# Kernel tuning notes

Measured on AMD Instinct MI355X. Metric: run time of the kernel, lower is better.

Reference implementation:

```python
import jax, jax.numpy as jnp
import numpy as np

DIM = 1024
HID = 2816
N_ROUTED = 7  # num_experts - num_shared_experts
TOPK = 2
B, S = 4, 2048


def _expert(x, wg, wu, wd):
    # DeepSeekExpertLayer: down(silu(gate(x)) * up(x)); weights stored [in, out]
    return (jax.nn.silu(x @ wg) * (x @ wu)) @ wd


def setup_inputs() -> dict:
    key = jax.random.key(0)
    ks = jax.random.split(key, 9)
    s = 0.02
    x = jax.random.normal(ks[0], (B, S, DIM), jnp.float32)
    shared_gate = jax.random.normal(ks[1], (DIM, HID), jnp.float32) * s
    shared_up = jax.random.normal(ks[2], (DIM, HID), jnp.float32) * s
    shared_down = jax.random.normal(ks[3], (HID, DIM), jnp.float32) * s
    routed_gate = jax.random.normal(ks[4], (N_ROUTED, DIM, HID), jnp.float32) * s
    routed_up = jax.random.normal(ks[5], (N_ROUTED, DIM, HID), jnp.float32) * s
    routed_down = jax.random.normal(ks[6], (N_ROUTED, HID, DIM), jnp.float32) * s
    Wr = jax.random.normal(ks[7], (DIM, N_ROUTED), jnp.float32) * s
    # NOTE: original inits routing_bias to zeros (degenerate routing since logits
    # are MULTIPLIED by it); use random values so routing is non-trivial.
    routing_bias = jax.random.normal(ks[8], (N_ROUTED,), jnp.float32)
    return dict(x=x, shared_gate=shared_gate, shared_up=shared_up, shared_down=shared_down,
                routed_gate=routed_gate, routed_up=routed_up, routed_down=routed_down,
                Wr=Wr, routing_bias=routing_bias)


def reference(x, shared_gate, shared_up, shared_down,
              routed_gate, routed_up, routed_down, Wr, routing_bias):
    b, s, d = x.shape
    n_exp = routed_gate.shape[0]
    # shared expert path (num_shared_experts == 1, no division)
    shared_out = _expert(x, shared_gate, shared_up, shared_down)
    # router: note logits are MULTIPLIED by routing_bias (faithful to source)
    logits = (x @ Wr) * routing_bias            # [b, s, E]
    probs = jax.nn.sigmoid(logits)
    scores, idx = jax.lax.top_k(probs, TOPK)    # [b, s, k]
    scores = scores / scores.sum(-1, keepdims=True)
    # per-token per-expert combine weight via scatter-add of top-k scores
    t = b * s
    xf = x.reshape(t, d)
    weights = jnp.zeros((t, n_exp), x.dtype).at[
        jnp.arange(t)[:, None], idx.reshape(t, TOPK)].add(scores.reshape(t, TOPK))
    combined = jnp.zeros_like(xf)
    for e in range(n_exp):  # static small loop over experts
        combined = combined + _expert(xf, routed_gate[e], routed_up[e], routed_down[e]) * weights[:, e:e + 1]
    return shared_out + combined.reshape(b, s, d)
```

## Files before the change

kernel.cpp:

```cpp
#include <hip/hip_runtime.h>
#include <hip/hip_bf16.h>

#define DIM 1024
#define HID 2816
#define NEXP 7
#define TOKENS 8192

#define MW_XB    0ull
#define MW_H     16777216ull
#define MW_WGU   114098176ull
#define MW_WD    206372864ull
#define MW_TOK   252510208ull
#define MW_WGT   252579328ull
#define MW_META  252648448ull
#define MW_NEED  252650496ull

typedef __bf16 bf16x8 __attribute__((ext_vector_type(8)));
typedef float f32x4 __attribute__((ext_vector_type(4)));

static __device__ __forceinline__ unsigned short f2b(float f) {
  union { float f; unsigned int i; } c; c.f = f;
  unsigned int i = c.i;
  unsigned int r = (i + 0x7fffu + ((i >> 16) & 1u)) >> 16;
  return (unsigned short)r;
}

static __device__ __forceinline__ void gload16(const void* g, void* l) {
  __builtin_amdgcn_global_load_lds(
      (const __attribute__((address_space(1))) unsigned int*)g,
      (__attribute__((address_space(3))) unsigned int*)l, 16, 0, 0);
}

__global__ __launch_bounds__(256, 2) void router_kernel(
    const float* __restrict__ X,
    const float* __restrict__ Wr,
    const float* __restrict__ bias,
    int* __restrict__ eidx,
    float* __restrict__ ew)
{
// ... 8 lines not shown
  for (int d0 = 0; d0 < DIM; d0 += 4) {
    float4 xv = *(const float4*)(xp + d0);
    const float* xs = (const float*)&xv;
#pragma unroll
    for (int j = 0; j < 4; ++j) {
      float xf = xs[j];
#pragma unroll
      for (int e = 0; e < NEXP; ++e) acc[e] += xf * wr[(d0 + j) * NEXP + e];
    }
  }
  float p[NEXP];
#pragma unroll
  for (int e = 0; e < NEXP; ++e)
    p[e] = 1.f / (1.f + __expf(-acc[e] * bias[e]));
  float best = -1.f; int bi = 0;
#pragma unroll
  for (int e = 0; e < NEXP; ++e) if (p[e] > best) { best = p[e]; bi = e; }
  float sec = -1.f; int si = 0;
#pragma unroll
  for (int e = 0; e < NEXP; ++e) if (e != bi && p[e] > sec) { sec = p[e]; si = e; }
  float s = best + sec;
  eidx[t] = bi | (si << 8);
  ((float2*)ew)[t] = make_float2(best / s, sec / s);
}

__global__ __launch_bounds__(256) void build_kernel(
    const int* __restrict__ eidx, const float* __restrict__ ew,
    int* __restrict__ tok, float* __restrict__ wgt, int* __restrict__ meta,
    int padmode)
{
  __shared__ int cnt[NEXP], fill[NEXP], ofs[NEXP];
  if (threadIdx.x < NEXP) { cnt[threadIdx.x] = 0; fill[threadIdx.x] = 0; }
  __syncthreads();
  for (int t = threadIdx.x; t < TOKENS; t += 256) {
    int p = eidx[t];
    atomicAdd(&cnt[p & 0xff], 1);
    atomicAdd(&cnt[(p >> 8) & 0xff], 1);
  }
  __syncthreads();
  if (threadIdx.x == 0) {
    int o = 0, nb = 0;
    for (int e = 0; e < NEXP; ++e) {
      ofs[e] = o;
      meta[e] = cnt[e];
      meta[8 + e] = o;
      if (padmode) {
        int b = (cnt[e] + 127) >> 7;
        for (int i = 0; i < b; ++i) meta[16 + nb++] = e | (i << 3);
        o += b << 7;
      } else {
        o += cnt[e];
      }
    }
    meta[15] = nb;
  }
  __syncthreads();
  for (int t = threadIdx.x; t < TOKENS; t += 256) {
    int p = eidx[t];
    int e0 = p & 0xff, e1 = (p >> 8) & 0xff;
    float2 w = ((const float2*)ew)[t];
    int p0 = ofs[e0] + atomicAdd(&fill[e0], 1);
    tok[p0] = t; wgt[p0] = w.x;
    int p1 = ofs[e1] + atomicAdd(&fill[e1], 1);
    tok[p1] = t; wgt[p1] = w.y;
  }
}

__global__ __launch_bounds__(256) void xcvt_kernel(
    const float* __restrict__ X, unsigned short* __restrict__ Xb)
{
  int i = (blockIdx.x * 256 + threadIdx.x) * 8;
  float4 v0 = *(const float4*)&X[i];
  float4 v1 = *(const float4*)&X[i + 4];
  unsigned short o[8];
  o[0] = f2b(v0.x); o[1] = f2b(v0.y); o[2] = f2b(v0.z); o[3] = f2b(v0.w);
  o[4] = f2b(v1.x); o[5] = f2b(v1.y); o[6] = f2b(v1.z); o[7] = f2b(v1.w);
  *(int4*)&Xb[i] = *(const int4*)o;
}

__global__ __launch_bounds__(256) void transpose_all_kernel(
    const float* __restrict__ sg, const float* __restrict__ su, const float* __restrict__ sd,
    const float* __restrict__ rg, const float* __restrict__ ru, const float* __restrict__ rd,
    unsigned short* __restrict__ WguA, unsigned short* __restrict__ WdA)
{
  int b = blockIdx.x;
  int e = b / 2112, r = b % 2112;
  int m = r / 704, q2 = r % 704;
  const float* src; unsigned short* dst; int K, N, nb, kb;
  if (m == 0) {
    src = e ? rg + (size_t)(e - 1) * DIM * HID : sg;
    dst = WguA + (size_t)e * (2 * (size_t)HID * DIM);
    K = DIM; N = HID; nb = q2 % 44; kb = q2 / 44;
  } else if (m == 1) {
    src = e ? ru + (size_t)(e - 1) * DIM * HID : su;
    dst = WguA + (size_t)e * (2 * (size_t)HID * DIM) + (size_t)HID * DIM;
    K = DIM; N = HID; nb = q2 % 44; kb = q2 / 44;
  } else {
    src = e ? rd + (size_t)(e - 1) * HID * DIM : sd;
    dst = WdA + (size_t)e * ((size_t)HID * DIM);
    K = HID; N = DIM; nb = q2 % 16; kb = q2 / 16;
  }
  __shared__ unsigned short t[64][72];
  const int n0 = nb * 64, k0 = kb * 64;
  const int tid = threadIdx.x;
  const int kl = tid >> 4, nl = (tid & 15) * 4;
#pragma unroll
  for (int i = 0; i < 4; ++i) {
    int k = kl + i * 16;
    float4 v = *(const float4*)&src[(size_t)(k0 + k) * N + n0 + nl];
    t[nl + 0][k] = f2b(v.x); t[nl + 1][k] = f2b(v.y);
    t[nl + 2][k] = f2b(v.z); t[nl + 3][k] = f2b(v.w);
  }
  __syncthreads();
  const int nl2 = tid >> 3, kc = (tid & 7) * 8;
#pragma unroll
  for (int i = 0; i < 2; ++i) {
    int n = nl2 + i * 32;
    *(int4*)&dst[(size_t)(n0 + n) * K + k0 + kc] = *(const int4*)&t[n][kc];
  }
}


__global__ __launch_bounds__(256, 2) void gateup_kernel(
    const unsigned short* __restrict__ Xb,
    const unsigned short* __restrict__ Wgu,
    unsigned short* __restrict__ H)
{
  __shared__ __align__(16) unsigned short As[128 * 64];
  __shared__ __align__(16) unsigned short Bgs[64 * 64];
  __shared__ __align__(16) unsigned short Bus[64 * 64];
  const int m0 = blockIdx.y * 128;
  const int n0 = blockIdx.x * 64;
  const int tid = threadIdx.x;
  const int lane = tid & 63;
  const int w = tid >> 6;
  const int wm = (w & 1) * 64;
  const int wn = (w >> 1) * 32;
  const int c = lane & 15;
  const int q = lane >> 4;
  const int cx = c & 7;

  const unsigned short* Wg = Wgu;
  const unsigned short* Wu = Wgu + (size_t)HID * DIM;

  const int r8 = lane >> 3;
  const int swz = ((lane & 7) ^ r8) * 8;
  const int wrow = w * 8 + r8;

  const unsigned short* aptr[4];
#pragma unroll
  for (int i = 0; i < 4; ++i)
    aptr[i] = Xb + (size_t)(m0 + i * 32 + wrow) * DIM + swz;
  const unsigned short* gptr[2];
  const unsigned short* uptr[2];
#pragma unroll
  for (int i = 0; i < 2; ++i) {
    gptr[i] = Wg + (size_t)(n0 + i * 32 + wrow) * DIM + swz;
    uptr[i] = Wu + (size_t)(n0 + i * 32 + wrow) * DIM + swz;
  }

  f32x4 accg[4][2], accu[4][2];
#pragma unroll
  for (int mi = 0; mi < 4; ++mi)
#pragma unroll
    for (int ni = 0; ni < 2; ++ni) {
      accg[mi][ni] = {0.f, 0.f, 0.f, 0.f};
      accu[mi][ni] = {0.f, 0.f, 0.f, 0.f};
    }

  for (int k0 = 0; k0 < DIM; k0 += 64) {
    __syncthreads();
#pragma unroll
    for (int i = 0; i < 4; ++i) gload16(aptr[i] + k0, &As[i * 2048 + tid * 8]);
#pragma unroll
    for (int i = 0; i < 2; ++i) {
      gload16(gptr[i] + k0, &Bgs[i * 2048 + tid * 8]);
      gload16(uptr[i] + k0, &Bus[i * 2048 + tid * 8]);
    }
    __syncthreads();
#pragma unroll
    for (int h = 0; h < 2; ++h) {
      const int go = ((h * 4 + q) ^ cx) * 8;
      bf16x8 a[4], bg[2], bu[2];
#pragma unroll
      for (int mi = 0; mi < 4; ++mi)
        a[mi] = *(const bf16x8*)&As[(wm + mi * 16 + c) * 64 + go];
#pragma unroll
      for (int ni = 0; ni < 2; ++ni) {
        bg[ni] = *(const bf16x8*)&Bgs[(wn + ni * 16 + c) * 64 + go];
        bu[ni] = *(const bf16x8*)&Bus[(wn + ni * 16 + c) * 64 + go];
      }
#pragma unroll
// ... 14 lines not shown
        int row = wm + mi * 16 + q * 4 + r;
        int col = wn + ni * 16 + c;
        float g = accg[mi][ni][r];
        float u = accu[mi][ni][r];
        float h = (g / (1.f + __expf(-g))) * u;
        H[(size_t)(m0 + row) * HID + n0 + col] = f2b(h);
      }
}

__global__ __launch_bounds__(256, 2) void gateup_sparse_all_kernel(
    const unsigned short* __restrict__ Xb,
    const unsigned short* __restrict__ WguR,
    const int* __restrict__ tok, const float* __restrict__ wgt,
    const int* __restrict__ meta,
    unsigned short* __restrict__ H)
{
  const int yb = blockIdx.y;
  if (yb >= meta[15]) return;
  const int bm = meta[16 + yb];
  const int e = bm & 7, mb = bm >> 3;
  const int cnt = meta[e];
  const int pofs = meta[8 + e];
  const unsigned short* Wgu = WguR + (size_t)e * (2 * (size_t)HID * DIM);

  __shared__ __align__(16) unsigned short As[128 * 64];
  __shared__ __align__(16) unsigned short Bgs[64 * 64];
  __shared__ __align__(16) unsigned short Bus[64 * 64];
  __shared__ float wl[128];

  const int n0 = blockIdx.x * 64;
  const int tid = threadIdx.x;
  const int lane = tid & 63;
  const int w = tid >> 6;
  const int wm = (w & 1) * 64;
  const int wn = (w >> 1) * 32;
  const int c = lane & 15;
  const int q = lane >> 4;
  const int cx = c & 7;

  if (tid < 128)
    wl[tid] = (mb * 128 + tid < cnt) ? wgt[pofs + mb * 128 + tid] : 0.f;

  const unsigned short* Wg = Wgu;
  const unsigned short* Wu = Wgu + (size_t)HID * DIM;

  const int r8 = lane >> 3;
  const int swz = ((lane & 7) ^ r8) * 8;
  const int wrow = w * 8 + r8;

  const unsigned short* aptr[4];
#pragma unroll
  for (int i = 0; i < 4; ++i) {
    int s = mb * 128 + i * 32 + wrow;
    int t = (s < cnt) ? tok[pofs + s] : 0;
    aptr[i] = Xb + (size_t)t * DIM + swz;
  }
  const unsigned short* gptr[2];
  const unsigned short* uptr[2];
#pragma unroll
  for (int i = 0; i < 2; ++i) {
    gptr[i] = Wg + (size_t)(n0 + i * 32 + wrow) * DIM + swz;
    uptr[i] = Wu + (size_t)(n0 + i * 32 + wrow) * DIM + swz;
  }

  f32x4 accg[4][2], accu[4][2];
#pragma unroll
  for (int mi = 0; mi < 4; ++mi)
#pragma unroll
    for (int ni = 0; ni < 2; ++ni) {
      accg[mi][ni] = {0.f, 0.f, 0.f, 0.f};
      accu[mi][ni] = {0.f, 0.f, 0.f, 0.f};
    }

  for (int k0 = 0; k0 < DIM; k0 += 64) {
    __syncthreads();
#pragma unroll
    for (int i = 0; i < 4; ++i) gload16(aptr[i] + k0, &As[i * 2048 + tid * 8]);
#pragma unroll
    for (int i = 0; i < 2; ++i) {
      gload16(gptr[i] + k0, &Bgs[i * 2048 + tid * 8]);
      gload16(uptr[i] + k0, &Bus[i * 2048 + tid * 8]);
    }
    __syncthreads();
#pragma unroll
    for (int h = 0; h < 2; ++h) {
      const int go = ((h * 4 + q) ^ cx) * 8;
      bf16x8 a[4], bg[2], bu[2];
#pragma unroll
      for (int mi = 0; mi < 4; ++mi)
        a[mi] = *(const bf16x8*)&As[(wm + mi * 16 + c) * 64 + go];
#pragma unroll
      for (int ni = 0; ni < 2; ++ni) {
        bg[ni] = *(const bf16x8*)&Bgs[(wn + ni * 16 + c) * 64 + go];
        bu[ni] = *(const bf16x8*)&Bus[(wn + ni * 16 + c) * 64 + go];
      }
#pragma unroll
// ... 17 lines not shown
        float u = accu[mi][ni][r];
        float h = (g / (1.f + __expf(-g))) * u * wl[row];
        H[(size_t)(pofs + mb * 128 + row) * HID + n0 + col] = f2b(h);
      }
}

__global__ __launch_bounds__(256, 2) void down_dense_kernel(
    const unsigned short* __restrict__ Hm,
    const unsigned short* __restrict__ WdT,
    float* __restrict__ out)
{
  __shared__ __align__(16) unsigned short As[128 * 64];
  __shared__ __align__(16) unsigned short Bs[128 * 64];
  const int m0 = blockIdx.y * 128;
  const int n0 = blockIdx.x * 128;
  const int tid = threadIdx.x;
  const int lane = tid & 63;
  const int w4 = tid >> 6;
  const int wm = (w4 & 1) * 64;
  const int wn = (w4 >> 1) * 64;
  const int c = lane & 15;
  const int q = lane >> 4;
  const int cx = c & 7;

  const int r8 = lane >> 3;
  const int swz = ((lane & 7) ^ r8) * 8;
  const int wrow = w4 * 8 + r8;

  const unsigned short* aptr[4];
  const unsigned short* bptr[4];
#pragma unroll
  for (int i = 0; i < 4; ++i) {
    aptr[i] = Hm + (size_t)(m0 + i * 32 + wrow) * HID + swz;
    bptr[i] = WdT + (size_t)(n0 + i * 32 + wrow) * HID + swz;
  }

  f32x4 acc[4][4];
#pragma unroll
  for (int mi = 0; mi < 4; ++mi)
#pragma unroll
    for (int ni = 0; ni < 4; ++ni) acc[mi][ni] = {0.f, 0.f, 0.f, 0.f};

  for (int k0 = 0; k0 < HID; k0 += 64) {
    __syncthreads();
#pragma unroll
    for (int i = 0; i < 4; ++i) {
      gload16(aptr[i] + k0, &As[i * 2048 + tid * 8]);
      gload16(bptr[i] + k0, &Bs[i * 2048 + tid * 8]);
    }
    __syncthreads();
#pragma unroll
    for (int h = 0; h < 2; ++h) {
      const int go = ((h * 4 + q) ^ cx) * 8;
      bf16x8 a[4], b[4];
#pragma unroll
      for (int mi = 0; mi < 4; ++mi)
        a[mi] = *(const bf16x8*)&As[(wm + mi * 16 + c) * 64 + go];
#pragma unroll
      for (int ni = 0; ni < 4; ++ni)
        b[ni] = *(const bf16x8*)&Bs[(wn + ni * 16 + c) * 64 + go];
#pragma unroll
      for (int mi = 0; mi < 4; ++mi)
#pragma unroll
        for (int ni = 0; ni < 4; ++ni)
          acc[mi][ni] = __builtin_amdgcn_mfma_f32_16x16x32_bf16(a[mi], b[ni], acc[mi][ni], 0, 0, 0);
// ... 6 lines not shown
      int trow = m0 + wm + mi * 16 + q * 4 + r;
#pragma unroll
      for (int ni = 0; ni < 4; ++ni) {
        int col = n0 + wn + ni * 16 + c;
        out[(size_t)trow * DIM + col] = acc[mi][ni][r];
      }
    }
}

__global__ __launch_bounds__(256, 2) void down_sparse_all_kernel(
    const unsigned short* __restrict__ Hm,
    const unsigned short* __restrict__ WdR,
    const int* __restrict__ tok, const int* __restrict__ meta,
    float* __restrict__ out)
{
  const int yb = blockIdx.y;
  if (yb >= meta[15]) return;
  const int bm = meta[16 + yb];
  const int e = bm & 7, mb = bm >> 3;
  const int cnt = meta[e];
  const int pofs = meta[8 + e];
  const unsigned short* WdT = WdR + (size_t)e * ((size_t)HID * DIM);
  const int kbase = blockIdx.z * (HID / 2);

  __shared__ __align__(16) unsigned short As[128 * 64];
  __shared__ __align__(16) unsigned short Bs[128 * 64];
  __shared__ int tl[128];
  const int n0 = blockIdx.x * 128;
  const int tid = threadIdx.x;
  const int lane = tid & 63;
  const int w4 = tid >> 6;
  const int wm = (w4 & 1) * 64;
  const int wn = (w4 >> 1) * 64;
  const int c = lane & 15;
  const int q = lane >> 4;
  const int cx = c & 7;

  if (tid < 128)
    tl[tid] = (mb * 128 + tid < cnt) ? tok[pofs + mb * 128 + tid] : 0;

  const int r8 = lane >> 3;
  const int swz = ((lane & 7) ^ r8) * 8;
  const int wrow = w4 * 8 + r8;

  const unsigned short* aptr[4];
  const unsigned short* bptr[4];
#pragma unroll
  for (int i = 0; i < 4; ++i) {
    aptr[i] = Hm + (size_t)(pofs + mb * 128 + i * 32 + wrow) * HID + kbase + swz;
    bptr[i] = WdT + (size_t)(n0 + i * 32 + wrow) * HID + kbase + swz;
  }

  f32x4 acc[4][4];
#pragma unroll
  for (int mi = 0; mi < 4; ++mi)
#pragma unroll
    for (int ni = 0; ni < 4; ++ni) acc[mi][ni] = {0.f, 0.f, 0.f, 0.f};

  for (int k0 = 0; k0 < HID / 2; k0 += 64) {
    __syncthreads();
#pragma unroll
    for (int i = 0; i < 4; ++i) {
      gload16(aptr[i] + k0, &As[i * 2048 + tid * 8]);
      gload16(bptr[i] + k0, &Bs[i * 2048 + tid * 8]);
    }
    __syncthreads();
#pragma unroll
    for (int h = 0; h < 2; ++h) {
      const int go = ((h * 4 + q) ^ cx) * 8;
      bf16x8 a[4], b[4];
#pragma unroll
      for (int mi = 0; mi < 4; ++mi)
        a[mi] = *(const bf16x8*)&As[(wm + mi * 16 + c) * 64 + go];
#pragma unroll
      for (int ni = 0; ni < 4; ++ni)
        b[ni] = *(const bf16x8*)&Bs[(wn + ni * 16 + c) * 64 + go];
#pragma unroll
      for (int mi = 0; mi < 4; ++mi)
#pragma unroll
        for (int ni = 0; ni < 4; ++ni)
          acc[mi][ni] = __builtin_amdgcn_mfma_f32_16x16x32_bf16(a[mi], b[ni], acc[mi][ni], 0, 0, 0);
    }
  }
#pragma unroll
  for (int mi = 0; mi < 4; ++mi)
#pragma unroll
    for (int r = 0; r < 4; ++r) {
      int lr = wm + mi * 16 + q * 4 + r;
      if (mb * 128 + lr < cnt) {
        int t = tl[lr];
#pragma unroll
        for (int ni = 0; ni < 4; ++ni) {
          int col = n0 + wn + ni * 16 + c;
          atomicAdd(&out[(size_t)t * DIM + col], acc[mi][ni][r]);
        }
      }
    }
}

__global__ __launch_bounds__(256, 2) void gateup_sparse_kernel(
    const unsigned short* __restrict__ Xb,
    const unsigned short* __restrict__ Wgu,
    const int* __restrict__ tok, const float* __restrict__ wgt,
    const int* __restrict__ cntofs, int e,
    unsigned short* __restrict__ H)
{
  const int cnt = cntofs[e];
  const int mb = blockIdx.y;
  if (mb * 128 >= cnt) return;
  const int ofs = cntofs[8 + e];

  __shared__ __align__(16) unsigned short As[128 * 64];
  __shared__ __align__(16) unsigned short Bgs[64 * 64];
  __shared__ __align__(16) unsigned short Bus[64 * 64];
  __shared__ float wl[128];

  const int n0 = blockIdx.x * 64;
  const int tid = threadIdx.x;
  const int lane = tid & 63;
  const int w = tid >> 6;
  const int wm = (w & 1) * 64;
  const int wn = (w >> 1) * 32;
  const int c = lane & 15;
  const int q = lane >> 4;
  const int cx = c & 7;

  if (tid < 128)
    wl[tid] = (mb * 128 + tid < cnt) ? wgt[ofs + mb * 128 + tid] : 0.f;

  const unsigned short* Wg = Wgu;
  const unsigned short* Wu = Wgu + (size_t)HID * DIM;

  const int r8 = lane >> 3;
  const int swz = ((lane & 7) ^ r8) * 8;
  const int wrow = w * 8 + r8;

  const unsigned short* aptr[4];
#pragma unroll
  for (int i = 0; i < 4; ++i) {
    int s = mb * 128 + i * 32 + wrow;
    int t = (s < cnt) ? tok[ofs + s] : 0;
    aptr[i] = Xb + (size_t)t * DIM + swz;
  }
  const unsigned short* gptr[2];
  const unsigned short* uptr[2];
#pragma unroll
  for (int i = 0; i < 2; ++i) {
    gptr[i] = Wg + (size_t)(n0 + i * 32 + wrow) * DIM + swz;
    uptr[i] = Wu + (size_t)(n0 + i * 32 + wrow) * DIM + swz;
  }

  f32x4 accg[4][2], accu[4][2];
#pragma unroll
  for (int mi = 0; mi < 4; ++mi)
#pragma unroll
    for (int ni = 0; ni < 2; ++ni) {
      accg[mi][ni] = {0.f, 0.f, 0.f, 0.f};
      accu[mi][ni] = {0.f, 0.f, 0.f, 0.f};
    }

  for (int k0 = 0; k0 < DIM; k0 += 64) {
    __syncthreads();
#pragma unroll
    for (int i = 0; i < 4; ++i) gload16(aptr[i] + k0, &As[i * 2048 + tid * 8]);
#pragma unroll
    for (int i = 0; i < 2; ++i) {
      gload16(gptr[i] + k0, &Bgs[i * 2048 + tid * 8]);
      gload16(uptr[i] + k0, &Bus[i * 2048 + tid * 8]);
    }
    __syncthreads();
#pragma unroll
    for (int h = 0; h < 2; ++h) {
      const int go = ((h * 4 + q) ^ cx) * 8;
      bf16x8 a[4], bg[2], bu[2];
#pragma unroll
      for (int mi = 0; mi < 4; ++mi)
        a[mi] = *(const bf16x8*)&As[(wm + mi * 16 + c) * 64 + go];
#pragma unroll
      for (int ni = 0; ni < 2; ++ni) {
        bg[ni] = *(const bf16x8*)&Bgs[(wn + ni * 16 + c) * 64 + go];
        bu[ni] = *(const bf16x8*)&Bus[(wn + ni * 16 + c) * 64 + go];
      }
#pragma unroll
      for (int mi = 0; mi < 4; ++mi)
#pragma unroll
        for (int ni = 0; ni < 2; ++ni) {
          accg[mi][ni] = __builtin_amdgcn_mfma_f32_16x16x32_bf16(a[mi], bg[ni], accg[mi][ni], 0, 0, 0);
          accu[mi][ni] = __builtin_amdgcn_mfma_f32_16x16x32_bf16(a[mi], bu[ni], accu[mi][ni], 0, 0, 0);
        }
    }
  }
#pragma unroll
  for (int mi = 0; mi < 4; ++mi)
#pragma unroll
    for (int ni = 0; ni < 2; ++ni)
#pragma unroll
      for (int r = 0; r < 4; ++r) {
        int row = wm + mi * 16 + q * 4 + r;
        int col = wn + ni * 16 + c;
        float g = accg[mi][ni][r];
        float u = accu[mi][ni][r];
        float h = (g / (1.f + __expf(-g))) * u * wl[row];
        H[(size_t)(mb * 128 + row) * HID + n0 + col] = f2b(h);
      }
}

__global__ __launch_bounds__(256, 2) void down_sparse_kernel(
    const unsigned short* __restrict__ Hm,
    const unsigned short* __restrict__ WdT,
    const int* __restrict__ tok, const int* __restrict__ cntofs, int e,
    float* __restrict__ out)
{
  const int cnt = cntofs[e];
  const int mb = blockIdx.y;
  if (mb * 128 >= cnt) return;
  const int ofs = cntofs[8 + e];
  const int kbase = blockIdx.z * (HID / 2);

  __shared__ __align__(16) unsigned short As[128 * 64];
  __shared__ __align__(16) unsigned short Bs[128 * 64];
  __shared__ int tl[128];
  const int n0 = blockIdx.x * 128;
  const int tid = threadIdx.x;
  const int lane = tid & 63;
  const int w4 = tid >> 6;
  const int wm = (w4 & 1) * 64;
  const int wn = (w4 >> 1) * 64;
  const int c = lane & 15;
  const int q = lane >> 4;
  const int cx = c & 7;

  if (tid < 128)
    tl[tid] = (mb * 128 + tid < cnt) ? tok[ofs + mb * 128 + tid] : 0;

  const int r8 = lane >> 3;
  const int swz = ((lane & 7) ^ r8) * 8;
  const int wrow = w4 * 8 + r8;

  const unsigned short* aptr[4];
  const unsigned short* bptr[4];
#pragma unroll
  for (int i = 0; i < 4; ++i) {
    aptr[i] = Hm + (size_t)(mb * 128 + i * 32 + wrow) * HID + kbase + swz;
    bptr[i] = WdT + (size_t)(n0 + i * 32 + wrow) * HID + kbase + swz;
  }

  f32x4 acc[4][4];
#pragma unroll
  for (int mi = 0; mi < 4; ++mi)
#pragma unroll
    for (int ni = 0; ni < 4; ++ni) acc[mi][ni] = {0.f, 0.f, 0.f, 0.f};

  for (int k0 = 0; k0 < HID / 2; k0 += 64) {
    __syncthreads();
#pragma unroll
    for (int i = 0; i < 4; ++i) {
      gload16(aptr[i] + k0, &As[i * 2048 + tid * 8]);
      gload16(bptr[i] + k0, &Bs[i * 2048 + tid * 8]);
    }
    __syncthreads();
#pragma unroll
    for (int h = 0; h < 2; ++h) {
      const int go = ((h * 4 + q) ^ cx) * 8;
      bf16x8 a[4], b[4];
#pragma unroll
      for (int mi = 0; mi < 4; ++mi)
        a[mi] = *(const bf16x8*)&As[(wm + mi * 16 + c) * 64 + go];
#pragma unroll
      for (int ni = 0; ni < 4; ++ni)
        b[ni] = *(const bf16x8*)&Bs[(wn + ni * 16 + c) * 64 + go];
#pragma unroll
      for (int mi = 0; mi < 4; ++mi)
#pragma unroll
        for (int ni = 0; ni < 4; ++ni)
          acc[mi][ni] = __builtin_amdgcn_mfma_f32_16x16x32_bf16(a[mi], b[ni], acc[mi][ni], 0, 0, 0);
// ... 13 lines not shown
        }
      }
    }
}

extern "C" void kernel_launch(void* const* d_in, const int* in_sizes, int n_in,
                              void* d_out, int out_size, void* d_ws, size_t ws_size,
                              hipStream_t stream) {
  (void)in_sizes; (void)n_in; (void)out_size;
  const float* x   = (const float*)d_in[0];
  const float* sg  = (const float*)d_in[1];
  const float* su  = (const float*)d_in[2];
  const float* sd  = (const float*)d_in[3];
  const float* rg  = (const float*)d_in[4];
  const float* ru  = (const float*)d_in[5];
  const float* rd  = (const float*)d_in[6];
  const float* wrr = (const float*)d_in[7];
  const float* rb  = (const float*)d_in[8];
  float* out = (float*)d_out;

  char* ws = (char*)d_ws;
  dim3 blk(256);

  if (ws_size >= MW_NEED) {
    unsigned short* Xb   = (unsigned short*)(ws + MW_XB);
    unsigned short* H    = (unsigned short*)(ws + MW_H);
    unsigned short* WguA = (unsigned short*)(ws + MW_WGU);
    unsigned short* WdA  = (unsigned short*)(ws + MW_WD);
    int*   tok           = (int*)(ws + MW_TOK);
    float* wgt           = (float*)(ws + MW_WGT);
    int*   meta          = (int*)(ws + MW_META);
    int*   eidx = (int*)H;
    float* ew   = (float*)((char*)H + 32768);

    router_kernel<<<dim3(TOKENS / 256), blk, 0, stream>>>(x, wrr, rb, eidx, ew);
    xcvt_kernel<<<dim3(TOKENS * DIM / (8 * 256)), blk, 0, stream>>>(x, Xb);
    build_kernel<<<dim3(1), blk, 0, stream>>>(eidx, ew, tok, wgt, meta, 1);
    transpose_all_kernel<<<dim3(8 * 2112), blk, 0, stream>>>(sg, su, sd, rg, ru, rd, WguA, WdA);

    gateup_kernel<<<dim3(HID / 64, TOKENS / 128), blk, 0, stream>>>(Xb, WguA, H);
    down_dense_kernel<<<dim3(DIM / 128, TOKENS / 128), blk, 0, stream>>>(H, WdA, out);

    const unsigned short* WguRt = WguA + 2 * (size_t)HID * DIM;
    const unsigned short* WdRt  = WdA + (size_t)HID * DIM;
    gateup_sparse_all_kernel<<<dim3(HID / 64, 135), blk, 0, stream>>>(Xb, WguRt, tok, wgt, meta, H);
    down_sparse_all_kernel<<<dim3(DIM / 128, 135, 2), blk, 0, stream>>>(H, WdRt, tok, meta, out);
  } else {
    unsigned short* Xb  = (unsigned short*)ws;
    unsigned short* H   = (unsigned short*)(ws + 16777216);
    unsigned short* Wgu = (unsigned short*)(ws + 62914560);
    unsigned short* Wd  = (unsigned short*)(ws + 74448896);
    int*   tok          = (int*)(ws + 80216064);
    float* wgt          = (float*)(ws + 80281600);
    int*   meta         = (int*)(ws + 80347136);
    int*   eidx = (int*)H;
    float* ew   = (float*)((char*)H + 32768);

    router_kernel<<<dim3(TOKENS / 256), blk, 0, stream>>>(x, wrr, rb, eidx, ew);
    xcvt_kernel<<<dim3(TOKENS * DIM / (8 * 256)), blk, 0, stream>>>(x, Xb);
    build_kernel<<<dim3(1), blk, 0, stream>>>(eidx, ew, tok, wgt, meta, 0);

    dim3 ggu(HID / 64, TOKENS / 128);
    dim3 gdn(DIM / 128, TOKENS / 128);
    dim3 gdns(DIM / 128, TOKENS / 128, 2);

    for (int e = 0; e < 8; ++e) {
      const float* eg = (e == 0) ? sg : rg + (size_t)(e - 1) * DIM * HID;
      const float* eu = (e == 0) ? su : ru + (size_t)(e - 1) * DIM * HID;
      const float* ed = (e == 0) ? sd : rd + (size_t)(e - 1) * HID * DIM;
      transpose_all_kernel<<<dim3(2112), blk, 0, stream>>>(eg, eu, ed, eg, eu, ed, Wgu, Wd);
      if (e == 0) {
        gateup_kernel<<<ggu, blk, 0, stream>>>(Xb, Wgu, H);
        down_dense_kernel<<<gdn, blk, 0, stream>>>(H, Wd, out);
      } else {
        gateup_sparse_kernel<<<ggu, blk, 0, stream>>>(Xb, Wgu, tok, wgt, meta, e - 1, H);
        down_sparse_kernel<<<gdns, blk, 0, stream>>>(H, Wd, tok, meta, e - 1, out);
      }
    }
  }
}
```

Before: 946.7 us.

## Unify shared and routed experts into single grouped GEMMs with deterministic combine

Treats the shared expert as expert 0 with an identity token list, so one grouped gate/up kernel and one grouped down kernel cover all experts. Workgroup IDs are remapped across XCDs so neighbouring tiles share weights in cache. The down GEMM now writes per-slot fp32 partials instead of atomically accumulating into the output, and a separate combine kernel sums the shared and two routed partials per token. A wave-ballot build kernel fills slot tables. This cuts launch count and atomic traffic, at the cost of a larger workspace and an extra fp32 partial write and read.

```diff
diff --git a/kernel.cpp b/kernel.cpp
--- a/kernel.cpp
+++ b/kernel.cpp
@@ -5,6 +5,16 @@
 #define HID 2816
 #define NEXP 7
 #define TOKENS 8192
+
+#define MW2_XB    0ull
+#define MW2_WGU   16777216ull
+#define MW2_WD    109051904ull
+#define MW2_H     155189248ull
+#define MW2_TOK   298647552ull
+#define MW2_WGT   298749440ull
+#define MW2_SLT   298851328ull
+#define MW2_META  298916864ull
+#define MW2_NEED  298918912ull
 
 #define MW_XB    0ull
 #define MW_H     16777216ull
@@ -15,6 +25,9 @@
 #define MW_META  252648448ull
 #define MW_NEED  252650496ull
 
+#define GU_NWG (44 * 199)
+#define DN_NWG (8 * 199)
+
 typedef __bf16 bf16x8 __attribute__((ext_vector_type(8)));
 typedef float f32x4 __attribute__((ext_vector_type(4)));
 
@@ -69,48 +82,6 @@
   float s = best + sec;
   eidx[t] = bi | (si << 8);
   ((float2*)ew)[t] = make_float2(best / s, sec / s);
-}
-
-__global__ __launch_bounds__(256) void build_kernel(
-    const int* __restrict__ eidx, const float* __restrict__ ew,
-    int* __restrict__ tok, float* __restrict__ wgt, int* __restrict__ meta,
-    int padmode)
-{
-  __shared__ int cnt[NEXP], fill[NEXP], ofs[NEXP];
-  if (threadIdx.x < NEXP) { cnt[threadIdx.x] = 0; fill[threadIdx.x] = 0; }
-  __syncthreads();
-  for (int t = threadIdx.x; t < TOKENS; t += 256) {
-    int p = eidx[t];
-    atomicAdd(&cnt[p & 0xff], 1);
-    atomicAdd(&cnt[(p >> 8) & 0xff], 1);
-  }
-  __syncthreads();
-  if (threadIdx.x == 0) {
-    int o = 0, nb = 0;
-    for (int e = 0; e < NEXP; ++e) {
-      ofs[e] = o;
-      meta[e] = cnt[e];
-      meta[8 + e] = o;
-      if (padmode) {
-        int b = (cnt[e] + 127) >> 7;
-        for (int i = 0; i < b; ++i) meta[16 + nb++] = e | (i << 3);
-        o += b << 7;
-      } else {
-        o += cnt[e];
-      }
-    }
-    meta[15] = nb;
-  }
-  __syncthreads();
-  for (int t = threadIdx.x; t < TOKENS; t += 256) {
-    int p = eidx[t];
-    int e0 = p & 0xff, e1 = (p >> 8) & 0xff;
-    float2 w = ((const float2*)ew)[t];
-    int p0 = ofs[e0] + atomicAdd(&fill[e0], 1);
-    tok[p0] = t; wgt[p0] = w.x;
-    int p1 = ofs[e1] + atomicAdd(&fill[e1], 1);
-    tok[p1] = t; wgt[p1] = w.y;
-  }
 }
 
 __global__ __launch_bounds__(256) void xcvt_kernel(
@@ -123,6 +94,75 @@
   o[0] = f2b(v0.x); o[1] = f2b(v0.y); o[2] = f2b(v0.z); o[3] = f2b(v0.w);
   o[4] = f2b(v1.x); o[5] = f2b(v1.y); o[6] = f2b(v1.z); o[7] = f2b(v1.w);
   *(int4*)&Xb[i] = *(const int4*)o;
+}
+
+__global__ __launch_bounds__(256) void build2_kernel(
+    const int* __restrict__ eidx, const float* __restrict__ ew,
+    int* __restrict__ tok, float* __restrict__ wgt,
+    int2* __restrict__ slt, int* __restrict__ meta)
+{
+  __shared__ int cnt[NEXP], fill[NEXP], ofs[NEXP];
+  const int tid = threadIdx.x;
+  const int lane = tid & 63, wid = tid >> 6;
+  if (tid < NEXP) { cnt[tid] = 0; fill[tid] = 0; }
+  for (int i = tid; i < TOKENS; i += 256) { tok[i] = i; wgt[i] = 1.f; }
+  __syncthreads();
+  const unsigned long long lmask = (1ull << lane) - 1ull;
+  for (int base = wid * 64; base < TOKENS; base += 256) {
+    int t = base + lane;
+    int p = eidx[t];
+    int e0 = p & 0xff, e1 = (p >> 8) & 0xff;
+#pragma unroll
+    for (int e = 0; e < NEXP; ++e) {
+      unsigned long long m0 = __ballot(e0 == e);
+      unsigned long long m1 = __ballot(e1 == e);
+      if (lane == 0) {
+        int tot = __popcll(m0) + __popcll(m1);
+        if (tot) atomicAdd(&cnt[e], tot);
+      }
+    }
+  }
+  __syncthreads();
+  if (tid == 0) {
+    int o = 0, nb = 0;
+    meta[0] = TOKENS; meta[8] = 0;
+    for (int i = 0; i < TOKENS / 128; ++i) meta[17 + nb++] = 0 | (i << 4);
+    for (int e = 0; e < NEXP; ++e) {
+      ofs[e] = o;
+      meta[1 + e] = cnt[e];
+      meta[9 + e] = TOKENS + o;
+      int b = (cnt[e] + 127) >> 7;
+      for (int i = 0; i < b; ++i) meta[17 + nb++] = (e + 1) | (i << 4);
+      o += b << 7;
+    }
+    meta[16] = nb;
+  }
+  __syncthreads();
+  for (int base = wid * 64; base < TOKENS; base += 256) {
+    int t = base + lane;
+    int p = eidx[t];
+    int e0 = p & 0xff, e1 = (p >> 8) & 0xff;
+    float2 w = ((const float2*)ew)[t];
+    int s0 = 0, s1 = 0;
+#pragma unroll
+    for (int e = 0; e < NEXP; ++e) {
+      unsigned long long m0 = __ballot(e0 == e);
+      unsigned long long m1 = __ballot(e1 == e);
+      int tot = __popcll(m0) + __popcll(m1);
+      int wb = 0;
+      if (lane == 0 && tot) wb = atomicAdd(&fill[e], tot);
+      wb = __shfl(wb, 0);
+      if (e0 == e) {
+        int sl = TOKENS + ofs[e] + wb + __popcll(m0 & lmask);
+        tok[sl] = t; wgt[sl] = w.x; s0 = sl;
+      }
+      if (e1 == e) {
+        int sl = TOKENS + ofs[e] + wb + __popcll(m0) + __popcll(m1 & lmask);
+        tok[sl] = t; wgt[sl] = w.y; s1 = sl;
+      }
+    }
+    slt[t] = make_int2(s0, s1);
+  }
 }
 
 __global__ __launch_bounds__(256) void transpose_all_kernel(
@@ -168,6 +208,260 @@
 }
 
 
+__global__ __launch_bounds__(256, 2) void gateup_all_kernel(
+    const unsigned short* __restrict__ Xb,
+    const unsigned short* __restrict__ WguA,
+    const int* __restrict__ tok, const float* __restrict__ wgt,
+    const int* __restrict__ meta,
+    unsigned short* __restrict__ H)
+{
+  const int q8 = GU_NWG / 8, r8g = GU_NWG % 8;
+  const int id = blockIdx.x;
+  const int xcd = id & 7, pos = id >> 3;
+  const int sid = (xcd < r8g ? xcd * (q8 + 1) : r8g * (q8 + 1) + (xcd - r8g) * q8) + pos;
+  const int yb = sid / 44, nblk = sid - yb * 44;
+  if (yb >= meta[16]) return;
+  const int ent = meta[17 + yb];
+  const int e = ent & 15, mb = ent >> 4;
+  const int cnt = meta[e];
+  const int pofs = meta[8 + e];
+  const unsigned short* Wg = WguA + (size_t)e * (2 * (size_t)HID * DIM);
+  const unsigned short* Wu = Wg + (size_t)HID * DIM;
+
+  __shared__ __align__(16) unsigned short As[128 * 64];
+  __shared__ __align__(16) unsigned short Bgs[64 * 64];
+  __shared__ __align__(16) unsigned short Bus[64 * 64];
+  __shared__ float wl[128];
+
+  const int n0 = nblk * 64;
+  const int tid = threadIdx.x;
+  const int lane = tid & 63;
+  const int w = tid >> 6;
+  const int wm = (w & 1) * 64;
+  const int wn = (w >> 1) * 32;
+  const int c = lane & 15;
+  const int q = lane >> 4;
+  const int cx = c & 7;
+
+  if (tid < 128)
+    wl[tid] = (mb * 128 + tid < cnt) ? wgt[pofs + mb * 128 + tid] : 0.f;
+
+  const int r8 = lane >> 3;
+  const int swz = ((lane & 7) ^ r8) * 8;
+  const int wrow = w * 8 + r8;
+
+  const unsigned short* aptr[4];
+#pragma unroll
+  for (int i = 0; i < 4; ++i) {
+    int s = mb * 128 + i * 32 + wrow;
+    int t = (s < cnt) ? tok[pofs + s] : 0;
+    aptr[i] = Xb + (size_t)t * DIM + swz;
+  }
+  const unsigned short* gptr[2];
+  const unsigned short* uptr[2];
+#pragma unroll
+  for (int i = 0; i < 2; ++i) {
+    gptr[i] = Wg + (size_t)(n0 + i * 32 + wrow) * DIM + swz;
+    uptr[i] = Wu + (size_t)(n0 + i * 32 + wrow) * DIM + swz;
+  }
+
+  f32x4 accg[4][2], accu[4][2];
+#pragma unroll
+  for (int mi = 0; mi < 4; ++mi)
+#pragma unroll
+    for (int ni = 0; ni < 2; ++ni) {
+      accg[mi][ni] = {0.f, 0.f, 0.f, 0.f};
+      accu[mi][ni] = {0.f, 0.f, 0.f, 0.f};
+    }
+
+  for (int k0 = 0; k0 < DIM; k0 += 64) {
+    __syncthreads();
+#pragma unroll
+    for (int i = 0; i < 4; ++i) gload16(aptr[i] + k0, &As[i * 2048 + tid * 8]);
+#pragma unroll
+    for (int i = 0; i < 2; ++i) {
+      gload16(gptr[i] + k0, &Bgs[i * 2048 + tid * 8]);
+      gload16(uptr[i] + k0, &Bus[i * 2048 + tid * 8]);
+    }
+    __syncthreads();
+#pragma unroll
+    for (int h = 0; h < 2; ++h) {
+      const int go = ((h * 4 + q) ^ cx) * 8;
+      bf16x8 a[4], bg[2], bu[2];
+#pragma unroll
+      for (int mi = 0; mi < 4; ++mi)
+        a[mi] = *(const bf16x8*)&As[(wm + mi * 16 + c) * 64 + go];
+#pragma unroll
+      for (int ni = 0; ni < 2; ++ni) {
+        bg[ni] = *(const bf16x8*)&Bgs[(wn + ni * 16 + c) * 64 + go];
+        bu[ni] = *(const bf16x8*)&Bus[(wn + ni * 16 + c) * 64 + go];
+      }
+#pragma unroll
+      for (int mi = 0; mi < 4; ++mi)
+#pragma unroll
+        for (int ni = 0; ni < 2; ++ni) {
+          accg[mi][ni] = __builtin_amdgcn_mfma_f32_16x16x32_bf16(a[mi], bg[ni], accg[mi][ni], 0, 0, 0);
+          accu[mi][ni] = __builtin_amdgcn_mfma_f32_16x16x32_bf16(a[mi], bu[ni], accu[mi][ni], 0, 0, 0);
+        }
+    }
+  }
+#pragma unroll
+  for (int mi = 0; mi < 4; ++mi)
+#pragma unroll
+    for (int ni = 0; ni < 2; ++ni)
+#pragma unroll
+      for (int r = 0; r < 4; ++r) {
+        int row = wm + mi * 16 + q * 4 + r;
+        int col = wn + ni * 16 + c;
+        float g = accg[mi][ni][r];
+        float u = accu[mi][ni][r];
+        float h = (g / (1.f + __expf(-g))) * u * wl[row];
+        H[(size_t)(pofs + mb * 128 + row) * HID + n0 + col] = f2b(h);
+      }
+}
+
+__global__ __launch_bounds__(256, 2) void down_all_kernel(
+    const unsigned short* __restrict__ Hm,
+    const unsigned short* __restrict__ WdA,
+    const int* __restrict__ meta,
+    float* __restrict__ P)
+{
+  const int q8 = DN_NWG / 8;
+  const int id = blockIdx.x;
+  const int sid = (id & 7) * q8 + (id >> 3);
+  const int yb = sid >> 3, nblk = sid & 7;
+  if (yb >= meta[16]) return;
+  const int ent = meta[17 + yb];
+  const int e = ent & 15, mb = ent >> 4;
+  const int pofs = meta[8 + e];
+  const unsigned short* WdT = WdA + (size_t)e * ((size_t)HID * DIM);
+
+  __shared__ __align__(16) unsigned short As[128 * 64];
+  __shared__ __align__(16) unsigned short Bs[128 * 64];
+  const int n0 = nblk * 128;
+  const int tid = threadIdx.x;
+  const int lane = tid & 63;
+  const int w4 = tid >> 6;
+  const int wm = (w4 & 1) * 64;
+  const int wn = (w4 >> 1) * 64;
+  const int c = lane & 15;
+  const int q = lane >> 4;
+  const int cx = c & 7;
+
+  const int r8 = lane >> 3;
+  const int swz = ((lane & 7) ^ r8) * 8;
+  const int wrow = w4 * 8 + r8;
+
+  const unsigned short* aptr[4];
+  const unsigned short* bptr[4];
+#pragma unroll
+  for (int i = 0; i < 4; ++i) {
+    aptr[i] = Hm + (size_t)(pofs + mb * 128 + i * 32 + wrow) * HID + swz;
+    bptr[i] = WdT + (size_t)(n0 + i * 32 + wrow) * HID + swz;
+  }
+
+  f32x4 acc[4][4];
+#pragma unroll
+  for (int mi = 0; mi < 4; ++mi)
+#pragma unroll
+    for (int ni = 0; ni < 4; ++ni) acc[mi][ni] = {0.f, 0.f, 0.f, 0.f};
+
+  for (int k0 = 0; k0 < HID; k0 += 64) {
+    __syncthreads();
+#pragma unroll
+    for (int i = 0; i < 4; ++i) {
+      gload16(aptr[i] + k0, &As[i * 2048 + tid * 8]);
+      gload16(bptr[i] + k0, &Bs[i * 2048 + tid * 8]);
+    }
+    __syncthreads();
+#pragma unroll
+    for (int h = 0; h < 2; ++h) {
+      const int go = ((h * 4 + q) ^ cx) * 8;
+      bf16x8 a[4], b[4];
+#pragma unroll
+      for (int mi = 0; mi < 4; ++mi)
+        a[mi] = *(const bf16x8*)&As[(wm + mi * 16 + c) * 64 + go];
+#pragma unroll
+      for (int ni = 0; ni < 4; ++ni)
+        b[ni] = *(const bf16x8*)&Bs[(wn + ni * 16 + c) * 64 + go];
+#pragma unroll
+      for (int mi = 0; mi < 4; ++mi)
+#pragma unroll
+        for (int ni = 0; ni < 4; ++ni)
+          acc[mi][ni] = __builtin_amdgcn_mfma_f32_16x16x32_bf16(a[mi], b[ni], acc[mi][ni], 0, 0, 0);
+    }
+  }
+#pragma unroll
+  for (int mi = 0; mi < 4; ++mi)
+#pragma unroll
+    for (int r = 0; r < 4; ++r) {
+      int prow = pofs + mb * 128 + wm + mi * 16 + q * 4 + r;
+#pragma unroll
+      for (int ni = 0; ni < 4; ++ni) {
+        int col = n0 + wn + ni * 16 + c;
+        P[(size_t)prow * DIM + col] = acc[mi][ni][r];
+      }
+    }
+}
+
+__global__ __launch_bounds__(256) void combine_kernel(
+    const float* __restrict__ P, const int2* __restrict__ slt,
+    float* __restrict__ out)
+{
+  const int t = blockIdx.x;
+  const int2 s = slt[t];
+  const int d = threadIdx.x;
+  float4 a = ((const float4*)(P + (size_t)t * DIM))[d];
+  float4 b = ((const float4*)(P + (size_t)s.x * DIM))[d];
+  float4 cc = ((const float4*)(P + (size_t)s.y * DIM))[d];
+  float4 o;
+  o.x = a.x + b.x + cc.x; o.y = a.y + b.y + cc.y;
+  o.z = a.z + b.z + cc.z; o.w = a.w + b.w + cc.w;
+  ((float4*)(out + (size_t)t * DIM))[d] = o;
+}
+
+__global__ __launch_bounds__(256) void build_kernel(
+    const int* __restrict__ eidx, const float* __restrict__ ew,
+    int* __restrict__ tok, float* __restrict__ wgt, int* __restrict__ meta,
+    int padmode)
+{
+  __shared__ int cnt[NEXP], fill[NEXP], ofs[NEXP];
+  if (threadIdx.x < NEXP) { cnt[threadIdx.x] = 0; fill[threadIdx.x] = 0; }
+  __syncthreads();
+  for (int t = threadIdx.x; t < TOKENS; t += 256) {
+    int p = eidx[t];
+    atomicAdd(&cnt[p & 0xff], 1);
+    atomicAdd(&cnt[(p >> 8) & 0xff], 1);
+  }
+  __syncthreads();
+  if (threadIdx.x == 0) {
+    int o = 0, nb = 0;
+    for (int e = 0; e < NEXP; ++e) {
+      ofs[e] = o;
+      meta[e] = cnt[e];
+      meta[8 + e] = o;
+      if (padmode) {
+        int b = (cnt[e] + 127) >> 7;
+        for (int i = 0; i < b; ++i) meta[16 + nb++] = e | (i << 3);
+        o += b << 7;
+      } else {
+        o += cnt[e];
+      }
+    }
+    meta[15] = nb;
+  }
+  __syncthreads();
+  for (int t = threadIdx.x; t < TOKENS; t += 256) {
+    int p = eidx[t];
+    int e0 = p & 0xff, e1 = (p >> 8) & 0xff;
+    float2 w = ((const float2*)ew)[t];
+    int p0 = ofs[e0] + atomicAdd(&fill[e0], 1);
+    tok[p0] = t; wgt[p0] = w.x;
+    int p1 = ofs[e1] + atomicAdd(&fill[e1], 1);
+    tok[p1] = t; wgt[p1] = w.y;
+  }
+}
+
 __global__ __launch_bounds__(256, 2) void gateup_kernel(
     const unsigned short* __restrict__ Xb,
     const unsigned short* __restrict__ Wgu,
@@ -186,14 +480,11 @@
   const int c = lane & 15;
   const int q = lane >> 4;
   const int cx = c & 7;
-
   const unsigned short* Wg = Wgu;
   const unsigned short* Wu = Wgu + (size_t)HID * DIM;
-
   const int r8 = lane >> 3;
   const int swz = ((lane & 7) ^ r8) * 8;
   const int wrow = w * 8 + r8;
-
   const unsigned short* aptr[4];
 #pragma unroll
   for (int i = 0; i < 4; ++i)
@@ -205,7 +496,6 @@
     gptr[i] = Wg + (size_t)(n0 + i * 32 + wrow) * DIM + swz;
     uptr[i] = Wu + (size_t)(n0 + i * 32 + wrow) * DIM + swz;
   }
-
   f32x4 accg[4][2], accu[4][2];
 #pragma unroll
   for (int mi = 0; mi < 4; ++mi)
@@ -214,7 +504,6 @@
       accg[mi][ni] = {0.f, 0.f, 0.f, 0.f};
       accu[mi][ni] = {0.f, 0.f, 0.f, 0.f};
     }
-
   for (int k0 = 0; k0 < DIM; k0 += 64) {
     __syncthreads();
 #pragma unroll
@@ -275,12 +564,10 @@
   const int cnt = meta[e];
   const int pofs = meta[8 + e];
   const unsigned short* Wgu = WguR + (size_t)e * (2 * (size_t)HID * DIM);
-
   __shared__ __align__(16) unsigned short As[128 * 64];
   __shared__ __align__(16) unsigned short Bgs[64 * 64];
   __shared__ __align__(16) unsigned short Bus[64 * 64];
   __shared__ float wl[128];
-
   const int n0 = blockIdx.x * 64;
   const int tid = threadIdx.x;
   const int lane = tid & 63;
@@ -290,17 +577,13 @@
   const int c = lane & 15;
   const int q = lane >> 4;
   const int cx = c & 7;
-
   if (tid < 128)
     wl[tid] = (mb * 128 + tid < cnt) ? wgt[pofs + mb * 128 + tid] : 0.f;
-
   const unsigned short* Wg = Wgu;
   const unsigned short* Wu = Wgu + (size_t)HID * DIM;
-
   const int r8 = lane >> 3;
   const int swz = ((lane & 7) ^ r8) * 8;
   const int wrow = w * 8 + r8;
-
   const unsigned short* aptr[4];
 #pragma unroll
   for (int i = 0; i < 4; ++i) {
@@ -315,7 +598,6 @@
     gptr[i] = Wg + (size_t)(n0 + i * 32 + wrow) * DIM + swz;
     uptr[i] = Wu + (size_t)(n0 + i * 32 + wrow) * DIM + swz;
   }
-
   f32x4 accg[4][2], accu[4][2];
 #pragma unroll
   for (int mi = 0; mi < 4; ++mi)
@@ -324,7 +606,6 @@
       accg[mi][ni] = {0.f, 0.f, 0.f, 0.f};
       accu[mi][ni] = {0.f, 0.f, 0.f, 0.f};
     }
-
   for (int k0 = 0; k0 < DIM; k0 += 64) {
     __syncthreads();
 #pragma unroll
@@ -388,11 +669,9 @@
   const int c = lane & 15;
   const int q = lane >> 4;
   const int cx = c & 7;
-
   const int r8 = lane >> 3;
   const int swz = ((lane & 7) ^ r8) * 8;
   const int wrow = w4 * 8 + r8;
-
   const unsigned short* aptr[4];
   const unsigned short* bptr[4];
 #pragma unroll
@@ -400,13 +679,11 @@
     aptr[i] = Hm + (size_t)(m0 + i * 32 + wrow) * HID + swz;
     bptr[i] = WdT + (size_t)(n0 + i * 32 + wrow) * HID + swz;
   }
-
   f32x4 acc[4][4];
 #pragma unroll
   for (int mi = 0; mi < 4; ++mi)
 #pragma unroll
     for (int ni = 0; ni < 4; ++ni) acc[mi][ni] = {0.f, 0.f, 0.f, 0.f};
-
   for (int k0 = 0; k0 < HID; k0 += 64) {
     __syncthreads();
 #pragma unroll
@@ -459,7 +736,6 @@
   const int pofs = meta[8 + e];
   const unsigned short* WdT = WdR + (size_t)e * ((size_t)HID * DIM);
   const int kbase = blockIdx.z * (HID / 2);
-
   __shared__ __align__(16) unsigned short As[128 * 64];
   __shared__ __align__(16) unsigned short Bs[128 * 64];
   __shared__ int tl[128];
@@ -472,14 +748,11 @@
   const int c = lane & 15;
   const int q = lane >> 4;
   const int cx = c & 7;
-
   if (tid < 128)
     tl[tid] = (mb * 128 + tid < cnt) ? tok[pofs + mb * 128 + tid] : 0;
-
   const int r8 = lane >> 3;
   const int swz = ((lane & 7) ^ r8) * 8;
   const int wrow = w4 * 8 + r8;
-
   const unsigned short* aptr[4];
   const unsigned short* bptr[4];
 #pragma unroll
@@ -487,207 +760,11 @@
     aptr[i] = Hm + (size_t)(pofs + mb * 128 + i * 32 + wrow) * HID + kbase + swz;
     bptr[i] = WdT + (size_t)(n0 + i * 32 + wrow) * HID + kbase + swz;
   }
-
   f32x4 acc[4][4];
 #pragma unroll
   for (int mi = 0; mi < 4; ++mi)
 #pragma unroll
     for (int ni = 0; ni < 4; ++ni) acc[mi][ni] = {0.f, 0.f, 0.f, 0.f};
-
-  for (int k0 = 0; k0 < HID / 2; k0 += 64) {
-    __syncthreads();
-#pragma unroll
-    for (int i = 0; i < 4; ++i) {
-      gload16(aptr[i] + k0, &As[i * 2048 + tid * 8]);
-      gload16(bptr[i] + k0, &Bs[i * 2048 + tid * 8]);
-    }
-    __syncthreads();
-#pragma unroll
-    for (int h = 0; h < 2; ++h) {
-      const int go = ((h * 4 + q) ^ cx) * 8;
-      bf16x8 a[4], b[4];
-#pragma unroll
-      for (int mi = 0; mi < 4; ++mi)
-        a[mi] = *(const bf16x8*)&As[(wm + mi * 16 + c) * 64 + go];
-#pragma unroll
-      for (int ni = 0; ni < 4; ++ni)
-        b[ni] = *(const bf16x8*)&Bs[(wn + ni * 16 + c) * 64 + go];
-#pragma unroll
-      for (int mi = 0; mi < 4; ++mi)
-#pragma unroll
-        for (int ni = 0; ni < 4; ++ni)
-          acc[mi][ni] = __builtin_amdgcn_mfma_f32_16x16x32_bf16(a[mi], b[ni], acc[mi][ni], 0, 0, 0);
-    }
-  }
-#pragma unroll
-  for (int mi = 0; mi < 4; ++mi)
-#pragma unroll
-    for (int r = 0; r < 4; ++r) {
-      int lr = wm + mi * 16 + q * 4 + r;
-      if (mb * 128 + lr < cnt) {
-        int t = tl[lr];
-#pragma unroll
-        for (int ni = 0; ni < 4; ++ni) {
-          int col = n0 + wn + ni * 16 + c;
-          atomicAdd(&out[(size_t)t * DIM + col], acc[mi][ni][r]);
-        }
-      }
-    }
-}
-
-__global__ __launch_bounds__(256, 2) void gateup_sparse_kernel(
-    const unsigned short* __restrict__ Xb,
-    const unsigned short* __restrict__ Wgu,
-    const int* __restrict__ tok, const float* __restrict__ wgt,
-    const int* __restrict__ cntofs, int e,
-    unsigned short* __restrict__ H)
-{
-  const int cnt = cntofs[e];
-  const int mb = blockIdx.y;
-  if (mb * 128 >= cnt) return;
-  const int ofs = cntofs[8 + e];
-
-  __shared__ __align__(16) unsigned short As[128 * 64];
-  __shared__ __align__(16) unsigned short Bgs[64 * 64];
-  __shared__ __align__(16) unsigned short Bus[64 * 64];
-  __shared__ float wl[128];
-
-  const int n0 = blockIdx.x * 64;
-  const int tid = threadIdx.x;
-  const int lane = tid & 63;
-  const int w = tid >> 6;
-  const int wm = (w & 1) * 64;
-  const int wn = (w >> 1) * 32;
-  const int c = lane & 15;
-  const int q = lane >> 4;
-  const int cx = c & 7;
-
-  if (tid < 128)
-    wl[tid] = (mb * 128 + tid < cnt) ? wgt[ofs + mb * 128 + tid] : 0.f;
-
-  const unsigned short* Wg = Wgu;
-  const unsigned short* Wu = Wgu + (size_t)HID * DIM;
-
-  const int r8 = lane >> 3;
-  const int swz = ((lane & 7) ^ r8) * 8;
-  const int wrow = w * 8 + r8;
-
-  const unsigned short* aptr[4];
-#pragma unroll
-  for (int i = 0; i < 4; ++i) {
-    int s = mb * 128 + i * 32 + wrow;
-    int t = (s < cnt) ? tok[ofs + s] : 0;
-    aptr[i] = Xb + (size_t)t * DIM + swz;
-  }
-  const unsigned short* gptr[2];
-  const unsigned short* uptr[2];
-#pragma unroll
-  for (int i = 0; i < 2; ++i) {
-    gptr[i] = Wg + (size_t)(n0 + i * 32 + wrow) * DIM + swz;
-    uptr[i] = Wu + (size_t)(n0 + i * 32 + wrow) * DIM + swz;
-  }
-
-  f32x4 accg[4][2], accu[4][2];
-#pragma unroll
-  for (int mi = 0; mi < 4; ++mi)
-#pragma unroll
-    for (int ni = 0; ni < 2; ++ni) {
-      accg[mi][ni] = {0.f, 0.f, 0.f, 0.f};
-      accu[mi][ni] = {0.f, 0.f, 0.f, 0.f};
-    }
-
-  for (int k0 = 0; k0 < DIM; k0 += 64) {
-    __syncthreads();
-#pragma unroll
-    for (int i = 0; i < 4; ++i) gload16(aptr[i] + k0, &As[i * 2048 + tid * 8]);
-#pragma unroll
-    for (int i = 0; i < 2; ++i) {
-      gload16(gptr[i] + k0, &Bgs[i * 2048 + tid * 8]);
-      gload16(uptr[i] + k0, &Bus[i * 2048 + tid * 8]);
-    }
-    __syncthreads();
-#pragma unroll
-    for (int h = 0; h < 2; ++h) {
-      const int go = ((h * 4 + q) ^ cx) * 8;
-      bf16x8 a[4], bg[2], bu[2];
-#pragma unroll
-      for (int mi = 0; mi < 4; ++mi)
-        a[mi] = *(const bf16x8*)&As[(wm + mi * 16 + c) * 64 + go];
-#pragma unroll
-      for (int ni = 0; ni < 2; ++ni) {
-        bg[ni] = *(const bf16x8*)&Bgs[(wn + ni * 16 + c) * 64 + go];
-        bu[ni] = *(const bf16x8*)&Bus[(wn + ni * 16 + c) * 64 + go];
-      }
-#pragma unroll
-      for (int mi = 0; mi < 4; ++mi)
-#pragma unroll
-        for (int ni = 0; ni < 2; ++ni) {
-          accg[mi][ni] = __builtin_amdgcn_mfma_f32_16x16x32_bf16(a[mi], bg[ni], accg[mi][ni], 0, 0, 0);
-          accu[mi][ni] = __builtin_amdgcn_mfma_f32_16x16x32_bf16(a[mi], bu[ni], accu[mi][ni], 0, 0, 0);
-        }
-    }
-  }
-#pragma unroll
-  for (int mi = 0; mi < 4; ++mi)
-#pragma unroll
-    for (int ni = 0; ni < 2; ++ni)
-#pragma unroll
-      for (int r = 0; r < 4; ++r) {
-        int row = wm + mi * 16 + q * 4 + r;
-        int col = wn + ni * 16 + c;
-        float g = accg[mi][ni][r];
-        float u = accu[mi][ni][r];
-        float h = (g / (1.f + __expf(-g))) * u * wl[row];
-        H[(size_t)(mb * 128 + row) * HID + n0 + col] = f2b(h);
-      }
-}
-
-__global__ __launch_bounds__(256, 2) void down_sparse_kernel(
-    const unsigned short* __restrict__ Hm,
-    const unsigned short* __restrict__ WdT,
-    const int* __restrict__ tok, const int* __restrict__ cntofs, int e,
-    float* __restrict__ out)
-{
-  const int cnt = cntofs[e];
-  const int mb = blockIdx.y;
-  if (mb * 128 >= cnt) return;
-  const int ofs = cntofs[8 + e];
-  const int kbase = blockIdx.z * (HID / 2);
-
-  __shared__ __align__(16) unsigned short As[128 * 64];
-  __shared__ __align__(16) unsigned short Bs[128 * 64];
-  __shared__ int tl[128];
-  const int n0 = blockIdx.x * 128;
-  const int tid = threadIdx.x;
-  const int lane = tid & 63;
-  const int w4 = tid >> 6;
-  const int wm = (w4 & 1) * 64;
-  const int wn = (w4 >> 1) * 64;
-  const int c = lane & 15;
-  const int q = lane >> 4;
-  const int cx = c & 7;
-
-  if (tid < 128)
-    tl[tid] = (mb * 128 + tid < cnt) ? tok[ofs + mb * 128 + tid] : 0;
-
-  const int r8 = lane >> 3;
-  const int swz = ((lane & 7) ^ r8) * 8;
-  const int wrow = w4 * 8 + r8;
-
-  const unsigned short* aptr[4];
-  const unsigned short* bptr[4];
-#pragma unroll
-  for (int i = 0; i < 4; ++i) {
-    aptr[i] = Hm + (size_t)(mb * 128 + i * 32 + wrow) * HID + kbase + swz;
-    bptr[i] = WdT + (size_t)(n0 + i * 32 + wrow) * HID + kbase + swz;
-  }
-
-  f32x4 acc[4][4];
-#pragma unroll
-  for (int mi = 0; mi < 4; ++mi)
-#pragma unroll
-    for (int ni = 0; ni < 4; ++ni) acc[mi][ni] = {0.f, 0.f, 0.f, 0.f};
-
   for (int k0 = 0; k0 < HID / 2; k0 += 64) {
     __syncthreads();
 #pragma unroll
@@ -747,7 +824,27 @@
   char* ws = (char*)d_ws;
   dim3 blk(256);
 
-  if (ws_size >= MW_NEED) {
+  if (ws_size >= MW2_NEED) {
+    unsigned short* Xb   = (unsigned short*)(ws + MW2_XB);
+    unsigned short* WguA = (unsigned short*)(ws + MW2_WGU);
+    unsigned short* WdA  = (unsigned short*)(ws + MW2_WD);
+    unsigned short* H    = (unsigned short*)(ws + MW2_H);
+    int*   tok           = (int*)(ws + MW2_TOK);
+    float* wgt           = (float*)(ws + MW2_WGT);
+    int2*  slt           = (int2*)(ws + MW2_SLT);
+    int*   meta          = (int*)(ws + MW2_META);
+    float* P             = (float*)ws;
+    int*   eidx = (int*)H;
+    float* ew   = (float*)((char*)H + 32768);
+
+    router_kernel<<<dim3(TOKENS / 256), blk, 0, stream>>>(x, wrr, rb, eidx, ew);
+    xcvt_kernel<<<dim3(TOKENS * DIM / (8 * 256)), blk, 0, stream>>>(x, Xb);
+    build2_kernel<<<dim3(1), blk, 0, stream>>>(eidx, ew, tok, wgt, slt, meta);
+    transpose_all_kernel<<<dim3(8 * 2112), blk, 0, stream>>>(sg, su, sd, rg, ru, rd, WguA, WdA);
+    gateup_all_kernel<<<dim3(GU_NWG), blk, 0, stream>>>(Xb, WguA, tok, wgt, meta, H);
+    down_all_kernel<<<dim3(DN_NWG), blk, 0, stream>>>(H, WdA, meta, P);
+    combine_kernel<<<dim3(TOKENS), blk, 0, stream>>>(P, slt, out);
+  } else {
     unsigned short* Xb   = (unsigned short*)(ws + MW_XB);
     unsigned short* H    = (unsigned short*)(ws + MW_H);
     unsigned short* WguA = (unsigned short*)(ws + MW_WGU);
@@ -762,45 +859,11 @@
     xcvt_kernel<<<dim3(TOKENS * DIM / (8 * 256)), blk, 0, stream>>>(x, Xb);
     build_kernel<<<dim3(1), blk, 0, stream>>>(eidx, ew, tok, wgt, meta, 1);
     transpose_all_kernel<<<dim3(8 * 2112), blk, 0, stream>>>(sg, su, sd, rg, ru, rd, WguA, WdA);
-
     gateup_kernel<<<dim3(HID / 64, TOKENS / 128), blk, 0, stream>>>(Xb, WguA, H);
     down_dense_kernel<<<dim3(DIM / 128, TOKENS / 128), blk, 0, stream>>>(H, WdA, out);
-
     const unsigned short* WguRt = WguA + 2 * (size_t)HID * DIM;
     const unsigned short* WdRt  = WdA + (size_t)HID * DIM;
     gateup_sparse_all_kernel<<<dim3(HID / 64, 135), blk, 0, stream>>>(Xb, WguRt, tok, wgt, meta, H);
     down_sparse_all_kernel<<<dim3(DIM / 128, 135, 2), blk, 0, stream>>>(H, WdRt, tok, meta, out);
-  } else {
-    unsigned short* Xb  = (unsigned short*)ws;
-    unsigned short* H   = (unsigned short*)(ws + 16777216);
-    unsigned short* Wgu = (unsigned short*)(ws + 62914560);
-    unsigned short* Wd  = (unsigned short*)(ws + 74448896);
-    int*   tok          = (int*)(ws + 80216064);
-    float* wgt          = (float*)(ws + 80281600);
-    int*   meta         = (int*)(ws + 80347136);
-    int*   eidx = (int*)H;
-    float* ew   = (float*)((char*)H + 32768);
-
-    router_kernel<<<dim3(TOKENS / 256), blk, 0, stream>>>(x, wrr, rb, eidx, ew);
-    xcvt_kernel<<<dim3(TOKENS * DIM / (8 * 256)), blk, 0, stream>>>(x, Xb);
-    build_kernel<<<dim3(1), blk, 0, stream>>>(eidx, ew, tok, wgt, meta, 0);
-
-    dim3 ggu(HID / 64, TOKENS / 128);
-    dim3 gdn(DIM / 128, TOKENS / 128);
-    dim3 gdns(DIM / 128, TOKENS / 128, 2);
-
-    for (int e = 0; e < 8; ++e) {
-      const float* eg = (e == 0) ? sg : rg + (size_t)(e - 1) * DIM * HID;
-      const float* eu = (e == 0) ? su : ru + (size_t)(e - 1) * DIM * HID;
-      const float* ed = (e == 0) ? sd : rd + (size_t)(e - 1) * HID * DIM;
-      transpose_all_kernel<<<dim3(2112), blk, 0, stream>>>(eg, eu, ed, eg, eu, ed, Wgu, Wd);
-      if (e == 0) {
-        gateup_kernel<<<ggu, blk, 0, stream>>>(Xb, Wgu, H);
-        down_dense_kernel<<<gdn, blk, 0, stream>>>(H, Wd, out);
-      } else {
-        gateup_sparse_kernel<<<ggu, blk, 0, stream>>>(Xb, Wgu, tok, wgt, meta, e - 1, H);
-        down_sparse_kernel<<<gdns, blk, 0, stream>>>(H, Wd, tok, meta, e - 1, out);
-      }
-    }
-  }
-}
+  }
+}
```

After: 970.5 us. 2.5% more time.
